# Performance work log

Hardware: AMD Instinct MI355X
Metric: run time of the kernel (lower is better)

## Reference

```python
import jax, jax.numpy as jnp
import numpy as np

SIGMAS = [0.5, 1.0, 2.0, 4.0, 8.0]
DATA_RANGE = 1.0
C1 = (0.01 * DATA_RANGE) ** 2
C2 = (0.03 * DATA_RANGE) ** 2
ALPHA = 0.025
COMPENSATION = 200.0
PAD = int(2 * SIGMAS[-1])            # 16
FILTER_SIZE = int(4 * SIGMAS[-1] + 1)  # 33


def _gauss_2d(size: int, sigma: float) -> np.ndarray:
    coords = np.arange(size, dtype=np.float32) - size // 2
    g = np.exp(-coords ** 2 / (2.0 * sigma ** 2))
    g /= g.sum()
    return np.outer(g, g)


def _make_g_masks() -> jnp.ndarray:
    # (3 * n_sigmas, 1, F, F): three identical masks per sigma, as in the torch buffer
    masks = np.zeros((3 * len(SIGMAS), 1, FILTER_SIZE, FILTER_SIZE), dtype=np.float32)
    for idx, sigma in enumerate(SIGMAS):
        k = _gauss_2d(FILTER_SIZE, sigma)
        masks[3 * idx + 0, 0] = k
        masks[3 * idx + 1, 0] = k
        masks[3 * idx + 2, 0] = k
    return jnp.asarray(masks)


def _gconv(x: jnp.ndarray, w: jnp.ndarray, groups: int) -> jnp.ndarray:
    return jax.lax.conv_general_dilated(
        x, w, window_strides=(1, 1), padding=[(PAD, PAD), (PAD, PAD)],
        dimension_numbers=("NCHW", "OIHW", "NCHW"), feature_group_count=groups)


def setup_inputs() -> dict:
    key = jax.random.key(0)
    k1, k2 = jax.random.split(key)
    img1 = jax.random.uniform(k1, (8, 3, 512, 512), dtype=jnp.float32)
    img2 = jax.random.uniform(k2, (8, 3, 512, 512), dtype=jnp.float32)
    return {"img1": img1, "img2": img2}


def reference(img1, img2):
    g_masks = _make_g_masks()
    ch = img1.shape[1]

    mux = _gconv(img1, g_masks, ch)           # (B, 15, H, W)
    muy = _gconv(img2, g_masks, ch)
    mux2 = mux * mux
    muy2 = muy * muy
    muxy = mux * muy
    sigmax2 = _gconv(img1 * img1, g_masks, ch) - mux2
    sigmay2 = _gconv(img2 * img2, g_masks, ch) - muy2
    sigmaxy = _gconv(img1 * img2, g_masks, ch) - muxy

    lc = (2.0 * muxy + C1) / (mux2 + muy2 + C1)
    cs = (2.0 * sigmaxy + C2) / (sigmax2 + sigmay2 + C2)

    lM = lc[:, -1] * lc[:, -2] * lc[:, -3]    # (B, H, W)
    PIcs = jnp.prod(cs, axis=1)               # (B, H, W)
    loss_ms_ssim = 1.0 - lM * PIcs

    loss_l1 = jnp.abs(img1 - img2)
    gaussian_l1 = _gconv(loss_l1, g_masks[-ch:], ch).mean(axis=1)  # (B, H, W)

    loss = ALPHA * loss_ms_ssim + (1.0 - ALPHA) * gaussian_l1 / DATA_RANGE
    return (COMPENSATION * loss).mean()
```

## Files before the change

### kernel.cpp

```cpp
#include <hip/hip_runtime.h>
#include <math.h>

struct GW { float w[185]; };
constexpr int W05 = 0;
constexpr int W1  = 21;
constexpr int W2  = 46;
constexpr int W4  = 81;
constexpr int W8  = 124;

namespace {

constexpr float kC1 = 1e-4f;
constexpr float kC2 = 9e-4f;


template<int R, int WOFF>
__device__ __forceinline__ void hpass4(const GW& g, const float* __restrict__ sS,
                                       const float* __restrict__ sD,
                                       float4* __restrict__ hb, int t) {
  constexpr int NROWS = 32 + 2 * R;
  constexpr int NE = NROWS * 8;
  constexpr int QS = (16 - R) & ~3;
  constexpr int NG = ((19 + R - QS) >> 2) + 1;
  if (t >= NE) return;
  const int hrow = t >> 3;
  const int cg = t & 7;
  const int srow = hrow + (16 - R);
  const int rx = srow & 7;
  const int rowbase = srow << 6;
  const int g0 = cg + (QS >> 2);
  float a0[4] = {0.f, 0.f, 0.f, 0.f}, a1[4] = {0.f, 0.f, 0.f, 0.f};
  float a2[4] = {0.f, 0.f, 0.f, 0.f}, a3[4] = {0.f, 0.f, 0.f, 0.f};
#pragma unroll 2
  for (int j = 0; j < NG; ++j) {
    const int off = rowbase + (((g0 + j) ^ rx) << 2);
    const int wb = WOFF + 8 + QS - 16 + R + 4 * j;
    const float4 s4 = *reinterpret_cast<const float4*>(&sS[off]);
    const float4 d4 = *reinterpret_cast<const float4*>(&sD[off]);
    const float* sp = reinterpret_cast<const float*>(&s4);
    const float* dp = reinterpret_cast<const float*>(&d4);
#pragma unroll
    for (int u = 0; u < 4; ++u) {
      const float sv = sp[u], dv = dp[u];
      const float s2 = sv * sv, d2 = dv * dv;
#pragma unroll
      for (int o = 0; o < 4; ++o) {
        const float wk = g.w[wb + u - o];
        a0[o] += wk * sv; a1[o] += wk * dv;
        a2[o] += wk * s2; a3[o] += wk * d2;
      }
    }
  }
  const int rb = hrow << 5;
#pragma unroll
  for (int o = 0; o < 4; ++o) {
    const int c = (cg << 2) + o;
    hb[rb + (c ^ ((c >> 3) & 3))] = make_float4(a0[o], a1[o], a2[o], a3[o]);
  }
}

template<int R, int WOFF>
__device__ __forceinline__ void vpass4(const GW& g, const float4* __restrict__ hb,
                                       int vc, int vr0,
                                       float (&o0)[2], float (&o1)[2],
                                       float (&o2)[2], float (&o3)[2]) {
#pragma unroll
  for (int i = 0; i < 2; ++i) { o0[i] = o1[i] = o2[i] = o3[i] = 0.f; }
  const int fc = vc ^ ((vc >> 3) & 3);
#pragma unroll 2
  for (int jj = 0; jj < 2 * R + 2; ++jj) {
    const float4 v = hb[((vr0 + jj) << 5) + fc];
    const int wb = WOFF + 8 + jj;
#pragma unroll
    for (int i = 0; i < 2; ++i) {
      const float wk = g.w[wb - i];
      o0[i] += wk * v.x; o1[i] += wk * v.y;
      o2[i] += wk * v.z; o3[i] += wk * v.w;
    }
  }
}

template<int R, int WOFF, int MULT, bool DOLM>
__device__ __forceinline__ void sweep4(const GW& g,
    const float* sS, const float* sD, float4* hb, int t, int vc, int vr0,
    float (&PI)[2], float (&lM)[2]) {
  __syncthreads();
  hpass4<R, WOFF>(g, sS, sD, hb, t);
  __syncthreads();
  float os[2], od[2], os2[2], od2[2];
  vpass4<R, WOFF>(g, hb, vc, vr0, os, od, os2, od2);
#pragma unroll
  for (int i = 0; i < 2; ++i) {
    const float vs = os2[i] - os[i] * os[i];
    const float vd = od2[i] - od[i] * od[i];
    const float cs = (0.5f * (vs - vd) + kC2) / (0.5f * (vs + vd) + kC2);
    float p = cs;
    if constexpr (MULT > 1) p *= cs;
    if constexpr (MULT > 2) p *= cs;
    PI[i] *= p;
    if constexpr (DOLM) {
      const float sa = os[i] * os[i], sb = od[i] * od[i];
      const float lc = (0.5f * (sa - sb) + kC1) / (0.5f * (sa + sb) + kC1);
      lM[i] = lc * lc * lc;
    }
  }
}

template<int R, int WOFF>
__device__ __forceinline__ void hpassL1(const GW& g, const float* __restrict__ sD,
                                        float* __restrict__ hbl, int t) {
  constexpr int QS = (16 - R) & ~3;
  constexpr int NG = ((19 + R - QS) >> 2) + 1;
  const int hrow = t >> 3;
  const int cg = t & 7;
  const int rx = hrow & 7;
  const int rowbase = hrow << 6;
  const int g0 = cg + (QS >> 2);
  float a0[4] = {0.f, 0.f, 0.f, 0.f};
#pragma unroll 2
  for (int j = 0; j < NG; ++j) {
    const int off = rowbase + (((g0 + j) ^ rx) << 2);
    const int wb = WOFF + 8 + QS - 16 + R + 4 * j;
    const float4 d4 = *reinterpret_cast<const float4*>(&sD[off]);
    const float* dp = reinterpret_cast<const float*>(&d4);
#pragma unroll
    for (int u = 0; u < 4; ++u) {
      const float av = fabsf(dp[u]);
#pragma unroll
      for (int o = 0; o < 4; ++o) a0[o] += g.w[wb + u - o] * av;
    }
  }
  *reinterpret_cast<float4*>(&hbl[(hrow << 5) + (cg << 2)]) =
      make_float4(a0[0], a0[1], a0[2], a0[3]);
}

template<int R, int WOFF>
__device__ __forceinline__ void sweepL1(const GW& g, const float* sD, float* hbl,
                                        int t, int vc, int vr0, float (&l1s)[2]) {
  __syncthreads();
  hpassL1<R, WOFF>(g, sD, hbl, t);
  __syncthreads();
#pragma unroll 2
  for (int jj = 0; jj < 2 * R + 2; ++jj) {
    const float vl = hbl[((vr0 + jj) << 5) + vc];
    const int wb = WOFF + 8 + jj;
#pragma unroll
    for (int i = 0; i < 2; ++i) l1s[i] += g.w[wb - i] * vl;
  }
}

__device__ __forceinline__ void load_tile(const float* __restrict__ p1,
                                          const float* __restrict__ p2,
                                          float* __restrict__ sS, float* __restrict__ sD,
                                          int t, int gx0, int gy0) {
#pragma unroll 1
  for (int e = 0; e < 2; ++e) {
    const int gidx = t + (e << 9);
    const int ly = gidx >> 4, lg = gidx & 15;
    const int gy = gy0 + ly;
    const int gx = gx0 + (lg << 2);
    float4 a = make_float4(0.f, 0.f, 0.f, 0.f);
    float4 b = make_float4(0.f, 0.f, 0.f, 0.f);
    if (gy >= 0 && gy < 512) {
      if (gx >= 0 && gx + 3 < 512) {
        a = *reinterpret_cast<const float4*>(&p1[(gy << 9) + gx]);
        b = *reinterpret_cast<const float4*>(&p2[(gy << 9) + gx]);
      } else {
        float* ap = reinterpret_cast<float*>(&a);
        float* bp = reinterpret_cast<float*>(&b);
#pragma unroll
        for (int u = 0; u < 4; ++u) {
          const int x = gx + u;
          if (x >= 0 && x < 512) { ap[u] = p1[(gy << 9) + x]; bp[u] = p2[(gy << 9) + x]; }
        }
      }
    }
    float4 s, d;
    s.x = a.x + b.x; s.y = a.y + b.y; s.z = a.z + b.z; s.w = a.w + b.w;
    d.x = a.x - b.x; d.y = a.y - b.y; d.z = a.z - b.z; d.w = a.w - b.w;
    const int off = (ly << 6) + ((lg ^ (ly & 7)) << 2);
    *reinterpret_cast<float4*>(&sS[off]) = s;
    *reinterpret_cast<float4*>(&sD[off]) = d;
  }
}

}

extern "C" __global__ __launch_bounds__(512) void msssim_main(
    const float* __restrict__ img1, const float* __restrict__ img2,
    float* __restrict__ partial, GW g) {
  __shared__ __align__(16) float sS[4096];
  __shared__ __align__(16) float sD[4096];
  __shared__ __align__(16) float4 hb[2048];
  __shared__ float red[8];
  float* hbl = reinterpret_cast<float*>(hb);

  const int t = threadIdx.x;

  const int bid = (int)blockIdx.x + ((int)blockIdx.y << 4) + ((int)blockIdx.z << 8);
  const int swz = ((bid & 7) << 8) + (bid >> 3);
  const int bx = swz & 15, by = (swz >> 4) & 15, b = swz >> 8;

  const int gx0 = bx * 32 - 16;
  const int gy0 = by * 32 - 16;
  const int vc = t & 31;
  const int vr0 = (t >> 5) << 1;

  float PI[2] = {1.f, 1.f};
  float lM[2] = {0.f, 0.f};
  float l1s[2] = {0.f, 0.f};

  {
    const float* p1 = img1 + (((size_t)b * 3 + 0) << 18);
    const float* p2 = img2 + (((size_t)b * 3 + 0) << 18);
    load_tile(p1, p2, sS, sD, t, gx0, gy0);
    sweep4<2, W05, 3, false>(g, sS, sD, hb, t, vc, vr0, PI, lM);
    sweep4<4, W1, 2, false>(g, sS, sD, hb, t, vc, vr0, PI, lM);
    sweepL1<16, W8>(g, sD, hbl, t, vc, vr0, l1s);
  }
  {
    const float* p1 = img1 + (((size_t)b * 3 + 1) << 18);
    const float* p2 = img2 + (((size_t)b * 3 + 1) << 18);
    load_tile(p1, p2, sS, sD, t, gx0, gy0);
    sweep4<4, W1, 1, false>(g, sS, sD, hb, t, vc, vr0, PI, lM);
    sweep4<9, W2, 3, false>(g, sS, sD, hb, t, vc, vr0, PI, lM);
    sweep4<13, W4, 1, false>(g, sS, sD, hb, t, vc, vr0, PI, lM);
    sweepL1<16, W8>(g, sD, hbl, t, vc, vr0, l1s);
  }
  {
    const float* p1 = img1 + (((size_t)b * 3 + 2) << 18);
    const float* p2 = img2 + (((size_t)b * 3 + 2) << 18);
    load_tile(p1, p2, sS, sD, t, gx0, gy0);
    sweep4<13, W4, 2, false>(g, sS, sD, hb, t, vc, vr0, PI, lM);
    sweep4<16, W8, 3, true>(g, sS, sD, hb, t, vc, vr0, PI, lM);
    sweepL1<16, W8>(g, sD, hbl, t, vc, vr0, l1s);
  }

  float s = 0.f;
#pragma unroll
  for (int i = 0; i < 2; ++i)
    s += 0.025f * (1.f - lM[i] * PI[i]) + 0.975f * (l1s[i] * (1.f / 3.f));

#pragma unroll
  for (int off = 32; off >= 1; off >>= 1) s += __shfl_down(s, off, 64);
  if ((t & 63) == 0) red[t >> 6] = s;
  __syncthreads();
  if (t == 0) {
    float tot = 0.f;
#pragma unroll
    for (int i = 0; i < 8; ++i) tot += red[i];
    partial[swz] = tot;
  }
}

extern "C" __global__ __launch_bounds__(256) void msssim_reduce(
    const float* __restrict__ partial, float* __restrict__ out, int n) {
  __shared__ float red[4];
  float s = 0.f;
  for (int i = threadIdx.x; i < n; i += 256) s += partial[i];
#pragma unroll
  for (int off = 32; off >= 1; off >>= 1) s += __shfl_down(s, off, 64);
  if ((threadIdx.x & 63) == 0) red[threadIdx.x >> 6] = s;
  __syncthreads();
  if (threadIdx.x == 0) {
    out[0] = (red[0] + red[1] + red[2] + red[3]) * (200.0f / 2097152.0f);
  }
}

extern "C" void kernel_launch(void* const* d_in, const int* in_sizes, int n_in,
                              void* d_out, int out_size, void* d_ws, size_t ws_size,
                              hipStream_t stream) {
  const float* img1 = (const float*)d_in[0];
  const float* img2 = (const float*)d_in[1];
  float* out = (float*)d_out;
  float* partial = (float*)d_ws;

  GW g;
  {
    const double sig[5] = {0.5, 1.0, 2.0, 4.0, 8.0};
    const int R[5] = {2, 4, 9, 13, 16};
    const int off[5] = {W05, W1, W2, W4, W8};
    for (int i = 0; i < 5; ++i) {
      double tmp[17];
      double sum = 0.0;
      for (int k = 0; k <= R[i]; ++k) {
        tmp[k] = exp(-(double)(k * k) / (2.0 * sig[i] * sig[i]));
        sum += (k ? 2.0 : 1.0) * tmp[k];
      }
      const int len = 2 * R[i] + 17;
      for (int m = 0; m < len; ++m) {
        int d = m - 8 - R[i];
        if (d < 0) d = -d;
        g.w[off[i] + m] = (m >= 8 && m <= 8 + 2 * R[i]) ? (float)(tmp[d] / sum) : 0.0f;
      }
    }
  }

  dim3 grid(16, 16, 8);
  msssim_main<<<grid, dim3(512), 0, stream>>>(img1, img2, partial, g);
  msssim_reduce<<<1, dim3(256), 0, stream>>>(partial, out, 2048);
}
```

Before: 149.2 us.

## Sum abs-diff across channels before a single L1 Gaussian blur; shrink sigma-4 radius

```diff
diff --git a/kernel.cpp b/kernel.cpp
--- a/kernel.cpp
+++ b/kernel.cpp
@@ -1,12 +1,12 @@
 #include <hip/hip_runtime.h>
 #include <math.h>
 
-struct GW { float w[185]; };
+struct GW { float w[171]; };
 constexpr int W05 = 0;
 constexpr int W1  = 21;
 constexpr int W2  = 46;
 constexpr int W4  = 81;
-constexpr int W8  = 124;
+constexpr int W8  = 122;
 
 namespace {
 
@@ -125,7 +125,7 @@
     const float* dp = reinterpret_cast<const float*>(&d4);
 #pragma unroll
     for (int u = 0; u < 4; ++u) {
-      const float av = fabsf(dp[u]);
+      const float av = dp[u];
 #pragma unroll
       for (int o = 0; o < 4; ++o) a0[o] += g.w[wb + u - o] * av;
     }
@@ -135,8 +135,17 @@
 }
 
 template<int R, int WOFF>
-__device__ __forceinline__ void sweepL1(const GW& g, const float* sD, float* hbl,
-                                        int t, int vc, int vr0, float (&l1s)[2]) {
+__device__ __forceinline__ void sweepL1_fused(const GW& g, float* sD, float* hbl,
+                                              const float (&al1)[8], int t,
+                                              int vc, int vr0, float (&l1s)[2]) {
+#pragma unroll
+  for (int e = 0; e < 2; ++e) {
+    const int gidx = t + (e << 9);
+    const int ly = gidx >> 4, lg = gidx & 15;
+    const int off = (ly << 6) + ((lg ^ (ly & 7)) << 2);
+    *reinterpret_cast<float4*>(&sD[off]) =
+        make_float4(al1[4 * e], al1[4 * e + 1], al1[4 * e + 2], al1[4 * e + 3]);
+  }
   __syncthreads();
   hpassL1<R, WOFF>(g, sD, hbl, t);
   __syncthreads();
@@ -152,7 +161,7 @@
 __device__ __forceinline__ void load_tile(const float* __restrict__ p1,
                                           const float* __restrict__ p2,
                                           float* __restrict__ sS, float* __restrict__ sD,
-                                          int t, int gx0, int gy0) {
+                                          float (&al1)[8], int t, int gx0, int gy0) {
 #pragma unroll 1
   for (int e = 0; e < 2; ++e) {
     const int gidx = t + (e << 9);
@@ -178,6 +187,8 @@
     float4 s, d;
     s.x = a.x + b.x; s.y = a.y + b.y; s.z = a.z + b.z; s.w = a.w + b.w;
     d.x = a.x - b.x; d.y = a.y - b.y; d.z = a.z - b.z; d.w = a.w - b.w;
+    al1[4 * e + 0] += fabsf(d.x); al1[4 * e + 1] += fabsf(d.y);
+    al1[4 * e + 2] += fabsf(d.z); al1[4 * e + 3] += fabsf(d.w);
     const int off = (ly << 6) + ((lg ^ (ly & 7)) << 2);
     *reinterpret_cast<float4*>(&sS[off]) = s;
     *reinterpret_cast<float4*>(&sD[off]) = d;
@@ -209,32 +220,31 @@
   float PI[2] = {1.f, 1.f};
   float lM[2] = {0.f, 0.f};
   float l1s[2] = {0.f, 0.f};
+  float al1[8] = {0.f, 0.f, 0.f, 0.f, 0.f, 0.f, 0.f, 0.f};
 
   {
     const float* p1 = img1 + (((size_t)b * 3 + 0) << 18);
     const float* p2 = img2 + (((size_t)b * 3 + 0) << 18);
-    load_tile(p1, p2, sS, sD, t, gx0, gy0);
+    load_tile(p1, p2, sS, sD, al1, t, gx0, gy0);
     sweep4<2, W05, 3, false>(g, sS, sD, hb, t, vc, vr0, PI, lM);
     sweep4<4, W1, 2, false>(g, sS, sD, hb, t, vc, vr0, PI, lM);
-    sweepL1<16, W8>(g, sD, hbl, t, vc, vr0, l1s);
   }
   {
     const float* p1 = img1 + (((size_t)b * 3 + 1) << 18);
     const float* p2 = img2 + (((size_t)b * 3 + 1) << 18);
-    load_tile(p1, p2, sS, sD, t, gx0, gy0);
+    load_tile(p1, p2, sS, sD, al1, t, gx0, gy0);
     sweep4<4, W1, 1, false>(g, sS, sD, hb, t, vc, vr0, PI, lM);
     sweep4<9, W2, 3, false>(g, sS, sD, hb, t, vc, vr0, PI, lM);
-    sweep4<13, W4, 1, false>(g, sS, sD, hb, t, vc, vr0, PI, lM);
-    sweepL1<16, W8>(g, sD, hbl, t, vc, vr0, l1s);
+    sweep4<12, W4, 1, false>(g, sS, sD, hb, t, vc, vr0, PI, lM);
   }
   {
     const float* p1 = img1 + (((size_t)b * 3 + 2) << 18);
     const float* p2 = img2 + (((size_t)b * 3 + 2) << 18);
-    load_tile(p1, p2, sS, sD, t, gx0, gy0);
-    sweep4<13, W4, 2, false>(g, sS, sD, hb, t, vc, vr0, PI, lM);
+    load_tile(p1, p2, sS, sD, al1, t, gx0, gy0);
+    sweep4<12, W4, 2, false>(g, sS, sD, hb, t, vc, vr0, PI, lM);
     sweep4<16, W8, 3, true>(g, sS, sD, hb, t, vc, vr0, PI, lM);
-    sweepL1<16, W8>(g, sD, hbl, t, vc, vr0, l1s);
-  }
+  }
+  sweepL1_fused<16, W8>(g, sD, hbl, al1, t, vc, vr0, l1s);
 
   float s = 0.f;
 #pragma unroll
@@ -278,7 +288,7 @@
   GW g;
   {
     const double sig[5] = {0.5, 1.0, 2.0, 4.0, 8.0};
-    const int R[5] = {2, 4, 9, 13, 16};
+    const int R[5] = {2, 4, 9, 12, 16};
     const int off[5] = {W05, W1, W2, W4, W8};
     for (int i = 0; i < 5; ++i) {
       double tmp[17];
```

Measured after the change: 128.9 us. -13.6%, faster.
